# Kernel tuning notes

Measured on AMD Instinct MI355X. Metric: run time of the kernel, lower is better.

The kernel has to match this reference:

```python
import jax, jax.numpy as jnp
import numpy as np

N_RES = 262144
C_S = 384
C_H = 128   # num_channels
N_BINS = 50


def setup_inputs() -> dict:
    key = jax.random.key(0)
    ks = jax.random.split(key, 9)
    s = lambda fan_in: 1.0 / np.sqrt(fan_in)
    return {
        "x": jax.random.normal(ks[0], (N_RES, C_S), dtype=jnp.float32),
        "ln_scale": jnp.ones((C_S,), dtype=jnp.float32),
        "ln_bias": jnp.zeros((C_S,), dtype=jnp.float32),
        "w0": jax.random.uniform(ks[1], (C_S, C_H), jnp.float32, -s(C_S), s(C_S)),
        "b0": jax.random.uniform(ks[2], (C_H,), jnp.float32, -s(C_S), s(C_S)),
        "w1": jax.random.uniform(ks[3], (C_H, C_H), jnp.float32, -s(C_H), s(C_H)),
        "b1": jax.random.uniform(ks[4], (C_H,), jnp.float32, -s(C_H), s(C_H)),
        "w2": jax.random.uniform(ks[5], (C_H, N_BINS), jnp.float32, -s(C_H), s(C_H)),
        "b2": jax.random.uniform(ks[6], (N_BINS,), jnp.float32, -s(C_H), s(C_H)),
    }


def _layer_norm(x, scale, bias, eps=1e-5):
    mu = jnp.mean(x, axis=-1, keepdims=True)
    var = jnp.mean(jnp.square(x - mu), axis=-1, keepdims=True)
    return (x - mu) * jax.lax.rsqrt(var + eps) * scale + bias


def reference(x, ln_scale, ln_bias, w0, b0, w1, b1, w2, b2):
    act = _layer_norm(x, ln_scale, ln_bias)            # [N_res, 384]
    act = jax.nn.relu(act @ w0 + b0)                   # [N_res, 128]
    act = jax.nn.relu(act @ w1 + b1)                   # [N_res, 128]
    logits = act @ w2 + b2                             # [N_res, 50]
    return logits
```

## Files before the change

### kernel.cpp

```cpp
#include <hip/hip_runtime.h>

typedef short bf16x8 __attribute__((ext_vector_type(8)));
typedef float f32x4 __attribute__((ext_vector_type(4)));

#define NRES 262144
#define BM 32

#define A0H 0
#define A0L 12544
#define AC0H 25088
#define AC0L 29440
#define A1H 0
#define A1L 12544
#define SMU 33792
#define A0_STR 392
#define ACT_STR 136

__device__ __forceinline__ unsigned short f2bf(float f) {
    unsigned u = __builtin_bit_cast(unsigned, f);
    u += 0x7FFFu + ((u >> 16) & 1u);
    return (unsigned short)(u >> 16);
}
__device__ __forceinline__ float bf2f(unsigned short h) {
    unsigned u = ((unsigned)h) << 16;
    return __builtin_bit_cast(float, u);
}

__device__ __forceinline__ void bfrag(const float* __restrict__ w, int ldw, int col, int k0,
                                      bf16x8& bh, bf16x8& bl) {
    union { unsigned u[4]; bf16x8 v; } H, L;
#pragma unroll
    for (int jj = 0; jj < 4; ++jj) {
        const float f0 = w[(k0 + 2 * jj)     * ldw + col];
        const float f1 = w[(k0 + 2 * jj + 1) * ldw + col];
        const unsigned short h0 = f2bf(f0), h1 = f2bf(f1);
        const unsigned short l0 = f2bf(f0 - bf2f(h0)), l1 = f2bf(f1 - bf2f(h1));
        H.u[jj] = (unsigned)h0 | ((unsigned)h1 << 16);
        L.u[jj] = (unsigned)l0 | ((unsigned)l1 << 16);
    }
    bh = H.v; bl = L.v;
}
__device__ __forceinline__ void bfrag50(const float* __restrict__ w, int col, int k0,
                                        bf16x8& bh, bf16x8& bl) {
    union { unsigned u[4]; bf16x8 v; } H, L;
    const bool ok = (col < 50);
#pragma unroll
    for (int jj = 0; jj < 4; ++jj) {
        const float f0 = ok ? w[(k0 + 2 * jj)     * 50 + col] : 0.0f;
        const float f1 = ok ? w[(k0 + 2 * jj + 1) * 50 + col] : 0.0f;
        const unsigned short h0 = f2bf(f0), h1 = f2bf(f1);
        const unsigned short l0 = f2bf(f0 - bf2f(h0)), l1 = f2bf(f1 - bf2f(h1));
        H.u[jj] = (unsigned)h0 | ((unsigned)h1 << 16);
        L.u[jj] = (unsigned)l0 | ((unsigned)l1 << 16);
    }
    bh = H.v; bl = L.v;
}

__global__ __launch_bounds__(256, 2)
void lddt_mfma(const float* __restrict__ x,
               const float* __restrict__ ln_scale,
               const float* __restrict__ ln_bias,
               const float* __restrict__ w0,
               const float* __restrict__ b0,
               const float* __restrict__ w1,
               const float* __restrict__ b1,
               const float* __restrict__ w2,
               const float* __restrict__ b2,
               float* __restrict__ out) {
    __shared__ __align__(16) unsigned short sm[SMU];

    const int tid  = threadIdx.x;
    const int lane = tid & 63;
    const int l15  = lane & 15;
    const int lg   = lane >> 4;
    const int wid  = tid >> 6;
    const long rowBase = (long)blockIdx.x * BM;

    {
        const float4* x4 = (const float4*)x;
        const int j = tid & 15;
#pragma unroll
        for (int rep = 0; rep < 2; ++rep) {
            const int row = rep * 16 + (tid >> 4);
            const long gr = rowBase + row;
            float4 v[6];
#pragma unroll
            for (int cs = 0; cs < 6; ++cs)
                v[cs] = x4[gr * 96 + cs * 16 + j];

            float s = 0.f, sq = 0.f;
#pragma unroll
            for (int cs = 0; cs < 6; ++cs) {
                s  += v[cs].x + v[cs].y + v[cs].z + v[cs].w;
                sq += v[cs].x*v[cs].x + v[cs].y*v[cs].y + v[cs].z*v[cs].z + v[cs].w*v[cs].w;
            }
#pragma unroll
            for (int d = 1; d < 16; d <<= 1) {
                s  += __shfl_xor(s,  d);
                sq += __shfl_xor(sq, d);
            }
            const float mu  = s * (1.0f / 384.0f);
            const float var = sq * (1.0f / 384.0f) - mu * mu;
            const float rs  = rsqrtf(var + 1e-5f);
#pragma unroll
            for (int cs = 0; cs < 6; ++cs) {
                const float4 sc = ((const float4*)ln_scale)[cs * 16 + j];
                const float4 bi = ((const float4*)ln_bias )[cs * 16 + j];
                float f[4];
                f[0] = (v[cs].x - mu) * rs * sc.x + bi.x;
                f[1] = (v[cs].y - mu) * rs * sc.y + bi.y;
                f[2] = (v[cs].z - mu) * rs * sc.z + bi.z;
                f[3] = (v[cs].w - mu) * rs * sc.w + bi.w;
                union { unsigned short h[4]; uint2 u; } ph, pl;
#pragma unroll
                for (int e = 0; e < 4; ++e) {
                    ph.h[e] = f2bf(f[e]);
                    pl.h[e] = f2bf(f[e] - bf2f(ph.h[e]));
                }
                const int idx = row * A0_STR + cs * 64 + j * 4;
                *(uint2*)&sm[A0H + idx] = ph.u;
                *(uint2*)&sm[A0L + idx] = pl.u;
            }
        }
    }
    __syncthreads();

    {
        f32x4 acc[2][2];
#pragma unroll
        for (int m = 0; m < 2; ++m) { acc[m][0] = (f32x4)0.0f; acc[m][1] = (f32x4)0.0f; }

#pragma unroll 4
        for (int s = 0; s < 12; ++s) {
            bf16x8 bh[2], bl[2], ah[2], al[2];
#pragma unroll
            for (int n = 0; n < 2; ++n)
                bfrag(w0, 128, wid * 32 + n * 16 + l15, s * 32 + lg * 8, bh[n], bl[n]);
#pragma unroll
            for (int m = 0; m < 2; ++m) {
                const int idx = (m * 16 + l15) * A0_STR + s * 32 + lg * 8;
                ah[m] = *(const bf16x8*)&sm[A0H + idx];
                al[m] = *(const bf16x8*)&sm[A0L + idx];
            }
#pragma unroll
            for (int m = 0; m < 2; ++m)
#pragma unroll
                for (int n = 0; n < 2; ++n) {
                    acc[m][n] = __builtin_amdgcn_mfma_f32_16x16x32_bf16(ah[m], bh[n], acc[m][n], 0, 0, 0);
                    acc[m][n] = __builtin_amdgcn_mfma_f32_16x16x32_bf16(ah[m], bl[n], acc[m][n], 0, 0, 0);
                    acc[m][n] = __builtin_amdgcn_mfma_f32_16x16x32_bf16(al[m], bh[n], acc[m][n], 0, 0, 0);
                }
        }
#pragma unroll
        for (int m = 0; m < 2; ++m)
#pragma unroll
            for (int n = 0; n < 2; ++n) {
                const int col = wid * 32 + n * 16 + l15;
                const float bb = b0[col];
#pragma unroll
                for (int r = 0; r < 4; ++r) {
                    const int row = m * 16 + lg * 4 + r;
                    const float z = fmaxf(acc[m][n][r] + bb, 0.0f);
                    const unsigned short h = f2bf(z);
                    const int idx = row * ACT_STR + col;
                    sm[AC0H + idx] = h;
                    sm[AC0L + idx] = f2bf(z - bf2f(h));
                }
            }
    }
    __syncthreads();

    {
        f32x4 acc[2][2];
#pragma unroll
        for (int m = 0; m < 2; ++m) { acc[m][0] = (f32x4)0.0f; acc[m][1] = (f32x4)0.0f; }

#pragma unroll
        for (int s = 0; s < 4; ++s) {
            bf16x8 bh[2], bl[2], ah[2], al[2];
#pragma unroll
            for (int n = 0; n < 2; ++n)
                bfrag(w1, 128, wid * 32 + n * 16 + l15, s * 32 + lg * 8, bh[n], bl[n]);
#pragma unroll
            for (int m = 0; m < 2; ++m) {
                const int idx = (m * 16 + l15) * ACT_STR + s * 32 + lg * 8;
                ah[m] = *(const bf16x8*)&sm[AC0H + idx];
                al[m] = *(const bf16x8*)&sm[AC0L + idx];
            }
#pragma unroll
            for (int m = 0; m < 2; ++m)
#pragma unroll
                for (int n = 0; n < 2; ++n) {
                    acc[m][n] = __builtin_amdgcn_mfma_f32_16x16x32_bf16(ah[m], bh[n], acc[m][n], 0, 0, 0);
                    acc[m][n] = __builtin_amdgcn_mfma_f32_16x16x32_bf16(ah[m], bl[n], acc[m][n], 0, 0, 0);
                    acc[m][n] = __builtin_amdgcn_mfma_f32_16x16x32_bf16(al[m], bh[n], acc[m][n], 0, 0, 0);
                }
        }
#pragma unroll
        for (int m = 0; m < 2; ++m)
#pragma unroll
            for (int n = 0; n < 2; ++n) {
                const int col = wid * 32 + n * 16 + l15;
                const float bb = b1[col];
#pragma unroll
                for (int r = 0; r < 4; ++r) {
                    const int row = m * 16 + lg * 4 + r;
                    const float z = fmaxf(acc[m][n][r] + bb, 0.0f);
                    const unsigned short h = f2bf(z);
                    const int idx = row * ACT_STR + col;
                    sm[A1H + idx] = h;
                    sm[A1L + idx] = f2bf(z - bf2f(h));
                }
            }
    }
    __syncthreads();

    {
        f32x4 acc[2];
        acc[0] = (f32x4)0.0f; acc[1] = (f32x4)0.0f;
        const int bcol = wid * 16 + l15;

#pragma unroll
        for (int s = 0; s < 4; ++s) {
            bf16x8 bh, bl, ah[2], al[2];
            bfrag50(w2, bcol, s * 32 + lg * 8, bh, bl);
#pragma unroll
            for (int m = 0; m < 2; ++m) {
                const int idx = (m * 16 + l15) * ACT_STR + s * 32 + lg * 8;
                ah[m] = *(const bf16x8*)&sm[A1H + idx];
                al[m] = *(const bf16x8*)&sm[A1L + idx];
            }
#pragma unroll
            for (int m = 0; m < 2; ++m) {
                acc[m] = __builtin_amdgcn_mfma_f32_16x16x32_bf16(ah[m], bh, acc[m], 0, 0, 0);
                acc[m] = __builtin_amdgcn_mfma_f32_16x16x32_bf16(ah[m], bl, acc[m], 0, 0, 0);
                acc[m] = __builtin_amdgcn_mfma_f32_16x16x32_bf16(al[m], bh, acc[m], 0, 0, 0);
            }
        }
        if (bcol < 50) {
            const float bb = b2[bcol];
#pragma unroll
            for (int m = 0; m < 2; ++m)
#pragma unroll
                for (int r = 0; r < 4; ++r) {
                    const long row = rowBase + m * 16 + lg * 4 + r;
                    out[row * 50 + bcol] = acc[m][r] + bb;
                }
        }
    }
}

extern "C" void kernel_launch(void* const* d_in, const int* in_sizes, int n_in,
                              void* d_out, int out_size, void* d_ws, size_t ws_size,
                              hipStream_t stream) {
    const float* x        = (const float*)d_in[0];
    const float* ln_scale = (const float*)d_in[1];
    const float* ln_bias  = (const float*)d_in[2];
    const float* w0       = (const float*)d_in[3];
    const float* b0       = (const float*)d_in[4];
    const float* w1       = (const float*)d_in[5];
    const float* b1       = (const float*)d_in[6];
    const float* w2       = (const float*)d_in[7];
    const float* b2       = (const float*)d_in[8];
    float* out = (float*)d_out;

    lddt_mfma<<<NRES / BM, 256, 0, stream>>>(
        x, ln_scale, ln_bias, w0, b0, w1, b1, w2, b2, out);
}
```

Measured before the change: 373.7 us.

## Pre-split weights into transposed bf16 hi/lo workspace with fallback kernel

Adds a prep kernel that converts w0/w1/w2 once per call into transposed bf16 hi/lo pairs in the workspace. The main kernel then loads ready-made 16-byte fragments instead of doing strided fp32 loads and bf16 splitting in every block. A check kernel and a flag let a fallback kernel run if the prepared data does not match. The extra launches (flag, prep, check, and an early-exit fallback grid) add fixed overhead per call. The layer-0 loop is also fully unrolled.

```diff
diff --git a/kernel.cpp b/kernel.cpp
--- a/kernel.cpp
+++ b/kernel.cpp
@@ -5,6 +5,16 @@
 
 #define NRES 262144
 #define BM 32
+#define GOODMAGIC 0x600DF00Du
+
+#define WT0H 0
+#define WT0L 49152
+#define WT1H 98304
+#define WT1L 114688
+#define WT2H 131072
+#define WT2L 139264
+#define PREP_N 73728
+#define WS_NEED ((size_t)(16 + PREP_N * 2 * 2))
 
 #define A0H 0
 #define A0L 12544
@@ -26,6 +36,250 @@
     return __builtin_bit_cast(float, u);
 }
 
+__global__ void set_flag(unsigned* flag, unsigned v) {
+    if (threadIdx.x == 0 && blockIdx.x == 0) *flag = v;
+}
+
+__device__ __forceinline__ void prep_index(int i, const float* w0, const float* w1,
+                                           const float* w2, float& v, int& hi_off, int& lo_off) {
+    if (i < 49152) {
+        int col = i / 384, k = i % 384;
+        v = w0[k * 128 + col]; hi_off = WT0H + i; lo_off = WT0L + i;
+    } else if (i < 65536) {
+        int j = i - 49152; int col = j / 128, k = j % 128;
+        v = w1[k * 128 + col]; hi_off = WT1H + j; lo_off = WT1L + j;
+    } else {
+        int j = i - 65536; int col = j / 128, k = j % 128;
+        v = (col < 50) ? w2[k * 50 + col] : 0.0f; hi_off = WT2H + j; lo_off = WT2L + j;
+    }
+}
+
+__global__ void prep_weights(const float* __restrict__ w0, const float* __restrict__ w1,
+                             const float* __restrict__ w2, unsigned short* __restrict__ wt) {
+    const int i = blockIdx.x * blockDim.x + threadIdx.x;
+    if (i >= PREP_N) return;
+    float v; int hi_off, lo_off;
+    prep_index(i, w0, w1, w2, v, hi_off, lo_off);
+    const unsigned short h = f2bf(v);
+    wt[hi_off] = h;
+    wt[lo_off] = f2bf(v - bf2f(h));
+}
+
+__global__ void check_weights(const float* __restrict__ w0, const float* __restrict__ w1,
+                              const float* __restrict__ w2, const unsigned short* __restrict__ wt,
+                              unsigned* flag) {
+    const int i = blockIdx.x * blockDim.x + threadIdx.x;
+    if (i >= PREP_N) return;
+    float v; int hi_off, lo_off;
+    prep_index(i, w0, w1, w2, v, hi_off, lo_off);
+    const unsigned short h = f2bf(v);
+    const unsigned short l = f2bf(v - bf2f(h));
+    if (wt[hi_off] != h || wt[lo_off] != l) atomicExch(flag, 0xBAD0BAD0u);
+}
+
+__device__ __forceinline__ void ln_phase(const float* __restrict__ x,
+                                         const float* __restrict__ ln_scale,
+                                         const float* __restrict__ ln_bias,
+                                         unsigned short* sm, int tid, long rowBase) {
+    const float4* x4 = (const float4*)x;
+    const int j = tid & 15;
+#pragma unroll
+    for (int rep = 0; rep < 2; ++rep) {
+        const int row = rep * 16 + (tid >> 4);
+        const long gr = rowBase + row;
+        float4 v[6];
+#pragma unroll
+        for (int cs = 0; cs < 6; ++cs)
+            v[cs] = x4[gr * 96 + cs * 16 + j];
+
+        float s = 0.f, sq = 0.f;
+#pragma unroll
+        for (int cs = 0; cs < 6; ++cs) {
+            s  += v[cs].x + v[cs].y + v[cs].z + v[cs].w;
+            sq += v[cs].x*v[cs].x + v[cs].y*v[cs].y + v[cs].z*v[cs].z + v[cs].w*v[cs].w;
+        }
+#pragma unroll
+        for (int d = 1; d < 16; d <<= 1) {
+            s  += __shfl_xor(s,  d);
+            sq += __shfl_xor(sq, d);
+        }
+        const float mu  = s * (1.0f / 384.0f);
+        const float var = sq * (1.0f / 384.0f) - mu * mu;
+        const float rs  = rsqrtf(var + 1e-5f);
+#pragma unroll
+        for (int cs = 0; cs < 6; ++cs) {
+            const float4 sc = ((const float4*)ln_scale)[cs * 16 + j];
+            const float4 bi = ((const float4*)ln_bias )[cs * 16 + j];
+            float f[4];
+            f[0] = (v[cs].x - mu) * rs * sc.x + bi.x;
+            f[1] = (v[cs].y - mu) * rs * sc.y + bi.y;
+            f[2] = (v[cs].z - mu) * rs * sc.z + bi.z;
+            f[3] = (v[cs].w - mu) * rs * sc.w + bi.w;
+            union { unsigned short h[4]; uint2 u; } ph, pl;
+#pragma unroll
+            for (int e = 0; e < 4; ++e) {
+                ph.h[e] = f2bf(f[e]);
+                pl.h[e] = f2bf(f[e] - bf2f(ph.h[e]));
+            }
+            const int idx = row * A0_STR + cs * 64 + j * 4;
+            *(uint2*)&sm[A0H + idx] = ph.u;
+            *(uint2*)&sm[A0L + idx] = pl.u;
+        }
+    }
+}
+
+__global__ __launch_bounds__(256, 2)
+void lddt_ws(const float* __restrict__ x,
+             const float* __restrict__ ln_scale,
+             const float* __restrict__ ln_bias,
+             const unsigned short* __restrict__ wt,
+             const unsigned* __restrict__ flag,
+             const float* __restrict__ b0,
+             const float* __restrict__ b1,
+             const float* __restrict__ b2,
+             float* __restrict__ out) {
+    if (*flag != GOODMAGIC) return;
+
+    __shared__ __align__(16) unsigned short sm[SMU];
+    const int tid  = threadIdx.x;
+    const int lane = tid & 63;
+    const int l15  = lane & 15;
+    const int lg   = lane >> 4;
+    const int wid  = tid >> 6;
+    const long rowBase = (long)blockIdx.x * BM;
+
+    ln_phase(x, ln_scale, ln_bias, sm, tid, rowBase);
+    __syncthreads();
+
+    {
+        f32x4 acc[2][2];
+#pragma unroll
+        for (int m = 0; m < 2; ++m) { acc[m][0] = (f32x4)0.0f; acc[m][1] = (f32x4)0.0f; }
+#pragma unroll
+        for (int s = 0; s < 12; ++s) {
+            bf16x8 bh[2], bl[2], ah[2], al[2];
+#pragma unroll
+            for (int n = 0; n < 2; ++n) {
+                const int bcol = wid * 32 + n * 16 + l15;
+                bh[n] = *(const bf16x8*)&wt[WT0H + bcol * 384 + s * 32 + lg * 8];
+                bl[n] = *(const bf16x8*)&wt[WT0L + bcol * 384 + s * 32 + lg * 8];
+            }
+#pragma unroll
+            for (int m = 0; m < 2; ++m) {
+                const int idx = (m * 16 + l15) * A0_STR + s * 32 + lg * 8;
+                ah[m] = *(const bf16x8*)&sm[A0H + idx];
+                al[m] = *(const bf16x8*)&sm[A0L + idx];
+            }
+#pragma unroll
+            for (int m = 0; m < 2; ++m)
+#pragma unroll
+                for (int n = 0; n < 2; ++n) {
+                    acc[m][n] = __builtin_amdgcn_mfma_f32_16x16x32_bf16(ah[m], bh[n], acc[m][n], 0, 0, 0);
+                    acc[m][n] = __builtin_amdgcn_mfma_f32_16x16x32_bf16(ah[m], bl[n], acc[m][n], 0, 0, 0);
+                    acc[m][n] = __builtin_amdgcn_mfma_f32_16x16x32_bf16(al[m], bh[n], acc[m][n], 0, 0, 0);
+                }
+        }
+#pragma unroll
+        for (int m = 0; m < 2; ++m)
+#pragma unroll
+            for (int n = 0; n < 2; ++n) {
+                const int col = wid * 32 + n * 16 + l15;
+                const float bb = b0[col];
+#pragma unroll
+                for (int r = 0; r < 4; ++r) {
+                    const int row = m * 16 + lg * 4 + r;
+                    const float z = fmaxf(acc[m][n][r] + bb, 0.0f);
+                    const unsigned short h = f2bf(z);
+                    const int idx = row * ACT_STR + col;
+                    sm[AC0H + idx] = h;
+                    sm[AC0L + idx] = f2bf(z - bf2f(h));
+                }
+            }
+    }
+    __syncthreads();
+
+    {
+        f32x4 acc[2][2];
+#pragma unroll
+        for (int m = 0; m < 2; ++m) { acc[m][0] = (f32x4)0.0f; acc[m][1] = (f32x4)0.0f; }
+#pragma unroll
+        for (int s = 0; s < 4; ++s) {
+            bf16x8 bh[2], bl[2], ah[2], al[2];
+#pragma unroll
+            for (int n = 0; n < 2; ++n) {
+                const int bcol = wid * 32 + n * 16 + l15;
+                bh[n] = *(const bf16x8*)&wt[WT1H + bcol * 128 + s * 32 + lg * 8];
+                bl[n] = *(const bf16x8*)&wt[WT1L + bcol * 128 + s * 32 + lg * 8];
+            }
+#pragma unroll
+            for (int m = 0; m < 2; ++m) {
+                const int idx = (m * 16 + l15) * ACT_STR + s * 32 + lg * 8;
+                ah[m] = *(const bf16x8*)&sm[AC0H + idx];
+                al[m] = *(const bf16x8*)&sm[AC0L + idx];
+            }
+#pragma unroll
+            for (int m = 0; m < 2; ++m)
+#pragma unroll
+                for (int n = 0; n < 2; ++n) {
+                    acc[m][n] = __builtin_amdgcn_mfma_f32_16x16x32_bf16(ah[m], bh[n], acc[m][n], 0, 0, 0);
+                    acc[m][n] = __builtin_amdgcn_mfma_f32_16x16x32_bf16(ah[m], bl[n], acc[m][n], 0, 0, 0);
+                    acc[m][n] = __builtin_amdgcn_mfma_f32_16x16x32_bf16(al[m], bh[n], acc[m][n], 0, 0, 0);
+                }
+        }
+#pragma unroll
+        for (int m = 0; m < 2; ++m)
+#pragma unroll
+            for (int n = 0; n < 2; ++n) {
+                const int col = wid * 32 + n * 16 + l15;
+                const float bb = b1[col];
+#pragma unroll
+                for (int r = 0; r < 4; ++r) {
+                    const int row = m * 16 + lg * 4 + r;
+                    const float z = fmaxf(acc[m][n][r] + bb, 0.0f);
+                    const unsigned short h = f2bf(z);
+                    const int idx = row * ACT_STR + col;
+                    sm[A1H + idx] = h;
+                    sm[A1L + idx] = f2bf(z - bf2f(h));
+                }
+            }
+    }
+    __syncthreads();
+
+    {
+        f32x4 acc[2];
+        acc[0] = (f32x4)0.0f; acc[1] = (f32x4)0.0f;
+        const int bcol = wid * 16 + l15;
+#pragma unroll
+        for (int s = 0; s < 4; ++s) {
+            bf16x8 bh, bl, ah[2], al[2];
+            bh = *(const bf16x8*)&wt[WT2H + bcol * 128 + s * 32 + lg * 8];
+            bl = *(const bf16x8*)&wt[WT2L + bcol * 128 + s * 32 + lg * 8];
+#pragma unroll
+            for (int m = 0; m < 2; ++m) {
+                const int idx = (m * 16 + l15) * ACT_STR + s * 32 + lg * 8;
+                ah[m] = *(const bf16x8*)&sm[A1H + idx];
+                al[m] = *(const bf16x8*)&sm[A1L + idx];
+            }
+#pragma unroll
+            for (int m = 0; m < 2; ++m) {
+                acc[m] = __builtin_amdgcn_mfma_f32_16x16x32_bf16(ah[m], bh, acc[m], 0, 0, 0);
+                acc[m] = __builtin_amdgcn_mfma_f32_16x16x32_bf16(ah[m], bl, acc[m], 0, 0, 0);
+                acc[m] = __builtin_amdgcn_mfma_f32_16x16x32_bf16(al[m], bh, acc[m], 0, 0, 0);
+            }
+        }
+        if (bcol < 50) {
+            const float bb = b2[bcol];
+#pragma unroll
+            for (int m = 0; m < 2; ++m)
+#pragma unroll
+                for (int r = 0; r < 4; ++r) {
+                    const long row = rowBase + m * 16 + lg * 4 + r;
+                    out[row * 50 + bcol] = acc[m][r] + bb;
+                }
+        }
+    }
+}
+
 __device__ __forceinline__ void bfrag(const float* __restrict__ w, int ldw, int col, int k0,
                                       bf16x8& bh, bf16x8& bl) {
     union { unsigned u[4]; bf16x8 v; } H, L;
@@ -57,7 +311,7 @@
 }
 
 __global__ __launch_bounds__(256, 2)
-void lddt_mfma(const float* __restrict__ x,
+void lddt_conv(const float* __restrict__ x,
                const float* __restrict__ ln_scale,
                const float* __restrict__ ln_bias,
                const float* __restrict__ w0,
@@ -66,9 +320,11 @@
                const float* __restrict__ b1,
                const float* __restrict__ w2,
                const float* __restrict__ b2,
+               const unsigned* flag,
                float* __restrict__ out) {
+    if (flag && *flag == GOODMAGIC) return;
+
     __shared__ __align__(16) unsigned short sm[SMU];
-
     const int tid  = threadIdx.x;
     const int lane = tid & 63;
     const int l15  = lane & 15;
@@ -76,61 +332,14 @@
     const int wid  = tid >> 6;
     const long rowBase = (long)blockIdx.x * BM;
 
-    {
-        const float4* x4 = (const float4*)x;
-        const int j = tid & 15;
-#pragma unroll
-        for (int rep = 0; rep < 2; ++rep) {
-            const int row = rep * 16 + (tid >> 4);
-            const long gr = rowBase + row;
-            float4 v[6];
-#pragma unroll
-            for (int cs = 0; cs < 6; ++cs)
-                v[cs] = x4[gr * 96 + cs * 16 + j];
-
-            float s = 0.f, sq = 0.f;
-#pragma unroll
-            for (int cs = 0; cs < 6; ++cs) {
-                s  += v[cs].x + v[cs].y + v[cs].z + v[cs].w;
-                sq += v[cs].x*v[cs].x + v[cs].y*v[cs].y + v[cs].z*v[cs].z + v[cs].w*v[cs].w;
-            }
-#pragma unroll
-            for (int d = 1; d < 16; d <<= 1) {
-                s  += __shfl_xor(s,  d);
-                sq += __shfl_xor(sq, d);
-            }
-            const float mu  = s * (1.0f / 384.0f);
-            const float var = sq * (1.0f / 384.0f) - mu * mu;
-            const float rs  = rsqrtf(var + 1e-5f);
-#pragma unroll
-            for (int cs = 0; cs < 6; ++cs) {
-                const float4 sc = ((const float4*)ln_scale)[cs * 16 + j];
-                const float4 bi = ((const float4*)ln_bias )[cs * 16 + j];
-                float f[4];
-                f[0] = (v[cs].x - mu) * rs * sc.x + bi.x;
-                f[1] = (v[cs].y - mu) * rs * sc.y + bi.y;
-                f[2] = (v[cs].z - mu) * rs * sc.z + bi.z;
-                f[3] = (v[cs].w - mu) * rs * sc.w + bi.w;
-                union { unsigned short h[4]; uint2 u; } ph, pl;
-#pragma unroll
-                for (int e = 0; e < 4; ++e) {
-                    ph.h[e] = f2bf(f[e]);
-                    pl.h[e] = f2bf(f[e] - bf2f(ph.h[e]));
-                }
-                const int idx = row * A0_STR + cs * 64 + j * 4;
-                *(uint2*)&sm[A0H + idx] = ph.u;
-                *(uint2*)&sm[A0L + idx] = pl.u;
-            }
-        }
-    }
+    ln_phase(x, ln_scale, ln_bias, sm, tid, rowBase);
     __syncthreads();
 
     {
         f32x4 acc[2][2];
 #pragma unroll
         for (int m = 0; m < 2; ++m) { acc[m][0] = (f32x4)0.0f; acc[m][1] = (f32x4)0.0f; }
-
-#pragma unroll 4
+#pragma unroll
         for (int s = 0; s < 12; ++s) {
             bf16x8 bh[2], bl[2], ah[2], al[2];
 #pragma unroll
@@ -174,7 +383,6 @@
         f32x4 acc[2][2];
 #pragma unroll
         for (int m = 0; m < 2; ++m) { acc[m][0] = (f32x4)0.0f; acc[m][1] = (f32x4)0.0f; }
-
 #pragma unroll
         for (int s = 0; s < 4; ++s) {
             bf16x8 bh[2], bl[2], ah[2], al[2];
@@ -219,7 +427,6 @@
         f32x4 acc[2];
         acc[0] = (f32x4)0.0f; acc[1] = (f32x4)0.0f;
         const int bcol = wid * 16 + l15;
-
 #pragma unroll
         for (int s = 0; s < 4; ++s) {
             bf16x8 bh, bl, ah[2], al[2];
@@ -264,6 +471,19 @@
     const float* b2       = (const float*)d_in[8];
     float* out = (float*)d_out;
 
-    lddt_mfma<<<NRES / BM, 256, 0, stream>>>(
-        x, ln_scale, ln_bias, w0, b0, w1, b1, w2, b2, out);
-}
+    const bool ws_ok = (ws_size >= WS_NEED);
+    if (ws_ok) {
+        unsigned* flag = (unsigned*)d_ws;
+        unsigned short* wt = (unsigned short*)d_ws + 8;
+        set_flag<<<1, 64, 0, stream>>>(flag, GOODMAGIC);
+        prep_weights<<<(PREP_N + 255) / 256, 256, 0, stream>>>(w0, w1, w2, wt);
+        check_weights<<<(PREP_N + 255) / 256, 256, 0, stream>>>(w0, w1, w2, wt, flag);
+        lddt_ws<<<NRES / BM, 256, 0, stream>>>(
+            x, ln_scale, ln_bias, wt, flag, b0, b1, b2, out);
+        lddt_conv<<<NRES / BM, 256, 0, stream>>>(
+            x, ln_scale, ln_bias, w0, b0, w1, b1, w2, b2, flag, out);
+    } else {
+        lddt_conv<<<NRES / BM, 256, 0, stream>>>(
+            x, ln_scale, ln_bias, w0, b0, w1, b1, w2, b2, (const unsigned*)nullptr, out);
+    }
+}
```

Result: faster. 347.5 us (median of 3 runs) (-7.0%).
